# Kernel optimization log

Hardware: AMD Instinct MI355X
Metric: run time of the kernel (lower is better)

## Reference

```python
import jax, jax.numpy as jnp
import numpy as np


def setup_inputs() -> dict:
    key = jax.random.key(0)
    k1, k2, k3 = jax.random.split(key, 3)
    x = jax.random.normal(k1, (8192, 2048), dtype=jnp.float32)
    w = jax.random.normal(k2, (4096, 2048), dtype=jnp.float32) * 0.02  # [out, in]
    b = jax.random.normal(k3, (4096,), dtype=jnp.float32) * 0.01
    return {"x": x, "w": w, "b": b}


def reference(x, w, b):
    # Straight-through binarization: forward uses sign(w), gradient flows as identity.
    binary_w = w + jax.lax.stop_gradient(jnp.sign(w) - w)  # [out, in], values in {-1, 0, 1}
    # F.linear: x @ W^T + b
    return jnp.einsum("ni,oi->no", x, binary_w) + b
```

## Files before the change

kernel.cpp:

```cpp
#include <hip/hip_runtime.h>
#include <hip/hip_bf16.h>
#include <stdint.h>

typedef __bf16 bf16x8 __attribute__((ext_vector_type(8)));
typedef float  f32x16 __attribute__((ext_vector_type(16)));


__device__ __forceinline__ uint32_t rn2_bf16(uint32_t lo, uint32_t hi) {
  uint32_t rlo = (lo + 0x7FFFu + ((lo >> 16) & 1u)) >> 16;
  uint32_t rhi = (hi + 0x7FFFu + ((hi >> 16) & 1u)) >> 16;
  return (rhi << 16) | (rlo & 0xFFFFu);
}

__device__ __forceinline__ uint32_t sign2_bf16(uint32_t lo, uint32_t hi) {
  uint32_t slo = (lo & 0x7FFFFFFFu) ? (0x3F80u | ((lo >> 16) & 0x8000u)) : 0u;
  uint32_t shi = (hi & 0x7FFFFFFFu) ? (0x3F80u | ((hi >> 16) & 0x8000u)) : 0u;
  return (shi << 16) | slo;
}

__device__ __forceinline__ void gl16(const void* g, void* l) {
  __builtin_amdgcn_global_load_lds(
      (const __attribute__((address_space(1))) uint32_t*)g,
      (__attribute__((address_space(3))) uint32_t*)l,
      16, 0, 0);
}


__global__ void prep_frag(const float* __restrict__ x, uint4* __restrict__ xf, int Mx,
                          const float* __restrict__ w, uint4* __restrict__ wf, int Nw,
                          int K) {
  const int kpw = K >> 6;
  const long nxc = ((long)Mx * K) >> 3;
  const long nwc = ((long)Nw * K) >> 3;
  const long stride = (long)gridDim.x * blockDim.x;
  for (long c = (long)blockIdx.x * blockDim.x + threadIdx.x; c < nxc + nwc; c += stride) {
    const bool isX = (c < nxc);
    const float* src = isX ? x : w;
    uint4* dst = isX ? xf : wf;
    const int rows32 = (isX ? Mx : Nw) >> 5;
    const long cc = isX ? c : (c - nxc);

    const int t = (int)(cc & 63);
    const long wv = cc >> 6;
    const int band = (int)(wv / kpw);
    const int kg = (int)(wv % kpw);
    const int row = band * 8 + (t & 7);
    const int k8 = kg * 8 + (t >> 3);

    const int kt = k8 >> 3, ks = (k8 >> 1) & 3, sub = k8 & 1;
    const int mb = row >> 5, r = row & 31;
    const long out16 = ((long)(kt * rows32 + mb) * 4 + ks) * 64 + sub * 32 + r;

    const uint4* s = reinterpret_cast<const uint4*>(src + (long)row * K + k8 * 8);
    uint4 a = s[0], b = s[1];
    uint4 o;
    if (isX) {
      o.x = rn2_bf16(a.x, a.y); o.y = rn2_bf16(a.z, a.w);
      o.z = rn2_bf16(b.x, b.y); o.w = rn2_bf16(b.z, b.w);
    } else {
      o.x = sign2_bf16(a.x, a.y); o.y = sign2_bf16(a.z, a.w);
      o.z = sign2_bf16(b.x, b.y); o.w = sign2_bf16(b.z, b.w);
    }
    dst[out16] = o;
  }
}


#define BARX()  asm volatile("s_barrier" ::: "memory")
#define VM0()   asm volatile("s_waitcnt vmcnt(0)" ::: "memory")
#define VMN4()  asm volatile("s_waitcnt vmcnt(4)" ::: "memory")

__global__ __launch_bounds__(512, 2) void gemm256(
    const uint16_t* __restrict__ Af,
    const uint16_t* __restrict__ Bf,
    const float* __restrict__ bias,
    float* __restrict__ C,
    int M, int N, int K) {
  __shared__ alignas(16) uint8_t L[131072];
  uint8_t* Lb = L;

  const int tid  = threadIdx.x;
  const int lane = tid & 63;
  const int w    = tid >> 6;
  const int wr   = w >> 2;
  const int wc   = w & 3;
  const int l31  = lane & 31;
  const int lhi  = lane >> 5;

  const int nbx = N >> 8;
  const int nwg = nbx * (M >> 8);
  const int bid = blockIdx.x;
  const int swb = (bid & 7) * (nwg >> 3) + (bid >> 3);
  const size_t m0 = (size_t)(swb / nbx) << 8;
  const size_t n0 = (size_t)(swb % nbx) << 8;

  const int NT = K >> 6;
  const size_t ktA = (size_t)(M >> 5) * 4096;
  const size_t ktB = (size_t)(N >> 5) * 4096;
  const char* Abase = (const char*)Af + (m0 >> 5) * 4096;
  const char* Bbase = (const char*)Bf + (n0 >> 5) * 4096;

  const int wB = w << 11;
  const int g0 = wB + lane * 16;
  const int g1 = g0 + 1024;

#define STG(LOFF, SRC) do { \
    gl16((SRC) + g0, Lb + (LOFF) + wB); \
    gl16((SRC) + g1, Lb + (LOFF) + wB + 1024); } while (0)

#define FRA32(d, i, q) (*reinterpret_cast<const bf16x8*>( \
    Lb + (d) * 65536 + wr * 16384 + (i) * 4096 + (q) * 1024 + lane * 16))
#define FRB32(d, j, q) (*reinterpret_cast<const bf16x8*>( \
    Lb + (d) * 65536 + 32768 + wc * 8192 + (j) * 4096 + (q) * 1024 + lane * 16))

#define RDA(DST, d, q) do { \
    _Pragma("unroll") \
    for (int i = 0; i < 4; ++i) DST[i] = FRA32(d, i, q); } while (0)
#define RDB(DST, d, q) do { \
    _Pragma("unroll") \
    for (int j = 0; j < 2; ++j) DST[j] = FRB32(d, j, q); } while (0)

  f32x16 acc[4][2] = {};

#define QM(A4, B2) do { \
    __builtin_amdgcn_s_setprio(1); \
    _Pragma("unroll") \
    for (int i = 0; i < 4; ++i) \
      _Pragma("unroll") \
      for (int j = 0; j < 2; ++j) \
        acc[i][j] = __builtin_amdgcn_mfma_f32_32x32x16_bf16( \
            A4[i], B2[j], acc[i][j], 0, 0, 0); \
    __builtin_amdgcn_s_setprio(0); } while (0)

  STG(0,      Abase);
  STG(16384,  Abase + 16384);
  STG(32768,  Bbase);
  STG(49152,  Bbase + 16384);
  STG(98304,  Bbase + ktB);
  STG(114688, Bbase + ktB + 16384);
  VMN4();
  BARX();

  bf16x8 aP[4], aQ[4], bP[2], bQ[2];
  RDA(aP, 0, 0);
  RDB(bP, 0, 0);

  const int T = K >> 7;
  for (int t = 0; t < T; ++t) {
    const int k2i = 2 * t + 2, k3i = 2 * t + 3;
    const char* A1 = Abase + (size_t)(2 * t + 1) * ktA;
    const char* A2 = Abase + (size_t)(k2i < NT ? k2i : NT - 1) * ktA;
    const char* B2 = Bbase + (size_t)(k2i < NT ? k2i : NT - 1) * ktB;
    const char* B3 = Bbase + (size_t)(k3i < NT ? k3i : NT - 1) * ktB;

    QM(aP, bP);
    RDA(aQ, 0, 1); RDB(bQ, 0, 1);
    STG(65536, A1);
    STG(81920, A1 + 16384);
    BARX();

    QM(aQ, bQ);
    RDA(aP, 0, 2); RDB(bP, 0, 2);
    BARX();

    QM(aP, bP);
    RDA(aQ, 0, 3); RDB(bQ, 0, 3);
    VM0();
    BARX();

    QM(aQ, bQ);
    RDA(aP, 1, 0); RDB(bP, 1, 0);
    STG(32768, B2);
    STG(49152, B2 + 16384);
    BARX();

    QM(aP, bP);
    RDA(aQ, 1, 1); RDB(bQ, 1, 1);
    STG(0, A2);
    STG(16384, A2 + 16384);
    BARX();

    QM(aQ, bQ);
    RDA(aP, 1, 2); RDB(bP, 1, 2);
    BARX();

    QM(aP, bP);
    RDA(aQ, 1, 3); RDB(bQ, 1, 3);
    VM0();
    BARX();

    QM(aQ, bQ);
    RDA(aP, 0, 0); RDB(bP, 0, 0);
    STG(98304, B3);
    STG(114688, B3 + 16384);
    BARX();
  }

#pragma unroll
  for (int i = 0; i < 4; ++i) {
#pragma unroll
    for (int j2 = 0; j2 < 2; ++j2) {
      const size_t col = n0 + wc * 64 + j2 * 32 + l31;
      const float bv = bias[col];
      const size_t rbase = m0 + wr * 128 + i * 32 + lhi * 4;
#pragma unroll
      for (int r = 0; r < 16; ++r) {
        const size_t row = rbase + (r & 3) + 8 * (r >> 2);
        C[row * N + col] = acc[i][j2][r] + bv;
      }
    }
  }
}

__global__ void gemm_naive(const float* __restrict__ x, const float* __restrict__ w,
                           const float* __restrict__ b, float* __restrict__ out,
                           int M, int N, int K) {
  int n = blockIdx.x * blockDim.x + threadIdx.x;
  int m = blockIdx.y;
  if (n >= N || m >= M) return;
  float acc = 0.f;
  for (int k = 0; k < K; ++k) {
    float wv = w[(size_t)n * K + k];
    float s = (wv > 0.f) ? 1.f : ((wv < 0.f) ? -1.f : 0.f);
    acc += x[(size_t)m * K + k] * s;
  }
  out[(size_t)m * N + n] = acc + b[n];
}

extern "C" void kernel_launch(void* const* d_in, const int* in_sizes, int n_in,
                              void* d_out, int out_size, void* d_ws, size_t ws_size,
                              hipStream_t stream) {
  const float* x = (const float*)d_in[0];
  const float* w = (const float*)d_in[1];
  const float* b = (const float*)d_in[2];
  float* out = (float*)d_out;

  const int N = in_sizes[2];
  const int K = in_sizes[1] / N;
  const int M = in_sizes[0] / K;

  const size_t need = ((size_t)M * K + (size_t)N * K) * sizeof(uint16_t);
  const bool big_ok = (M % 256 == 0) && (N % 256 == 0) && (K % 256 == 0) &&
                      (((M / 256) * (N / 256)) % 8 == 0) && (ws_size >= need);
  if (!big_ok) {
    hipLaunchKernelGGL(gemm_naive, dim3((N + 255) / 256, M), dim3(256), 0, stream,
                       x, w, b, out, M, N, K);
    return;
  }

  uint16_t* Xf = (uint16_t*)d_ws;
  uint16_t* Wf = Xf + (size_t)M * K;

  hipLaunchKernelGGL(prep_frag, dim3(2048), dim3(256), 0, stream,
                     x, (uint4*)Xf, M, w, (uint4*)Wf, N, K);

  hipLaunchKernelGGL(gemm256, dim3((M / 256) * (N / 256)), dim3(512), 0, stream,
                     Xf, Wf, b, out, M, N, K);
}
```

Measured before the change: 145.4 us.

## Deepen register fragment prefetch to two steps and rebalance LDS staging schedule

Reworks the main loop's software pipeline so LDS fragment reads run two sub-steps ahead using four register buffers instead of two. Global-to-LDS staging of the next A and B tiles is redistributed across the eight phases, and the prologue now preloads the second A tile. The aim is to hide LDS read latency behind more MFMA work and spread global loads more evenly. The cost is higher register pressure, which could hurt occupancy under the 2-blocks-per-SM launch bound, and a final vmcnt wait is added after the loop.

```diff
diff --git a/kernel.cpp b/kernel.cpp
--- a/kernel.cpp
+++ b/kernel.cpp
@@ -68,7 +68,7 @@
 
 #define BARX()  asm volatile("s_barrier" ::: "memory")
 #define VM0()   asm volatile("s_waitcnt vmcnt(0)" ::: "memory")
-#define VMN4()  asm volatile("s_waitcnt vmcnt(4)" ::: "memory")
+#define VMN8()  asm volatile("s_waitcnt vmcnt(8)" ::: "memory")
 
 __global__ __launch_bounds__(512, 2) void gemm256(
     const uint16_t* __restrict__ Af,
@@ -136,65 +136,68 @@
   STG(16384,  Abase + 16384);
   STG(32768,  Bbase);
   STG(49152,  Bbase + 16384);
+  STG(65536,  Abase + ktA);
+  STG(81920,  Abase + ktA + 16384);
   STG(98304,  Bbase + ktB);
   STG(114688, Bbase + ktB + 16384);
-  VMN4();
+  VMN8();
   BARX();
 
-  bf16x8 aP[4], aQ[4], bP[2], bQ[2];
-  RDA(aP, 0, 0);
-  RDB(bP, 0, 0);
-
-  const int T = K >> 7;
-  for (int t = 0; t < T; ++t) {
-    const int k2i = 2 * t + 2, k3i = 2 * t + 3;
-    const char* A1 = Abase + (size_t)(2 * t + 1) * ktA;
-    const char* A2 = Abase + (size_t)(k2i < NT ? k2i : NT - 1) * ktA;
-    const char* B2 = Bbase + (size_t)(k2i < NT ? k2i : NT - 1) * ktB;
-    const char* B3 = Bbase + (size_t)(k3i < NT ? k3i : NT - 1) * ktB;
-
-    QM(aP, bP);
-    RDA(aQ, 0, 1); RDB(bQ, 0, 1);
-    STG(65536, A1);
-    STG(81920, A1 + 16384);
-    BARX();
-
-    QM(aQ, bQ);
-    RDA(aP, 0, 2); RDB(bP, 0, 2);
-    BARX();
-
-    QM(aP, bP);
-    RDA(aQ, 0, 3); RDB(bQ, 0, 3);
+  bf16x8 S0a[4], S0b[2], S1a[4], S1b[2], S2a[4], S2b[2], S3a[4], S3b[2];
+  RDA(S0a, 0, 0); RDB(S0b, 0, 0);
+  RDA(S1a, 0, 1); RDB(S1b, 0, 1);
+
+  const int T2 = K >> 7;
+  for (int t = 0; t < T2; ++t) {
+    const int u2 = 2 * t + 2, u3 = 2 * t + 3;
+    const char* A2 = Abase + (size_t)(u2 < NT ? u2 : NT - 1) * ktA;
+    const char* B2 = Bbase + (size_t)(u2 < NT ? u2 : NT - 1) * ktB;
+    const char* A3 = Abase + (size_t)(u3 < NT ? u3 : NT - 1) * ktA;
+    const char* B3 = Bbase + (size_t)(u3 < NT ? u3 : NT - 1) * ktB;
+
+    QM(S0a, S0b);
+    RDA(S2a, 0, 2); RDB(S2b, 0, 2);
+    BARX();
+
+    QM(S1a, S1b);
+    RDA(S3a, 0, 3); RDB(S3b, 0, 3);
     VM0();
     BARX();
 
-    QM(aQ, bQ);
-    RDA(aP, 1, 0); RDB(bP, 1, 0);
+    QM(S2a, S2b);
+    RDA(S0a, 1, 0); RDB(S0b, 1, 0);
+    STG(0, A2);
+    STG(16384, A2 + 16384);
+    BARX();
+
+    QM(S3a, S3b);
+    RDA(S1a, 1, 1); RDB(S1b, 1, 1);
     STG(32768, B2);
     STG(49152, B2 + 16384);
     BARX();
 
-    QM(aP, bP);
-    RDA(aQ, 1, 1); RDB(bQ, 1, 1);
-    STG(0, A2);
-    STG(16384, A2 + 16384);
-    BARX();
-
-    QM(aQ, bQ);
-    RDA(aP, 1, 2); RDB(bP, 1, 2);
-    BARX();
-
-    QM(aP, bP);
-    RDA(aQ, 1, 3); RDB(bQ, 1, 3);
+    QM(S0a, S0b);
+    RDA(S2a, 1, 2); RDB(S2b, 1, 2);
+    BARX();
+
+    QM(S1a, S1b);
+    RDA(S3a, 1, 3); RDB(S3b, 1, 3);
     VM0();
     BARX();
 
-    QM(aQ, bQ);
-    RDA(aP, 0, 0); RDB(bP, 0, 0);
+    QM(S2a, S2b);
+    RDA(S0a, 0, 0); RDB(S0b, 0, 0);
+    STG(65536, A3);
+    STG(81920, A3 + 16384);
+    BARX();
+
+    QM(S3a, S3b);
+    RDA(S1a, 0, 1); RDB(S1b, 0, 1);
     STG(98304, B3);
     STG(114688, B3 + 16384);
     BARX();
   }
+  VM0();
 
 #pragma unroll
   for (int i = 0; i < 4; ++i) {
```

New measurement: 145.9 us. No clear change (+0.4%).
